# Kernel optimization log

Measured on AMD Instinct MI355X. Metric: run time of the kernel, lower is better.

Reference implementation:

```python
import jax, jax.numpy as jnp
import numpy as np

W_CD = 1.0   # cfg TRAIN.LOSS_WEIGHT_CHAMFER_DISTANCE
W_RV = 1.0   # cfg TRAIN.LOSS_WEIGHT_RANGE_VIEW
W_MASK = 1.0 # cfg TRAIN.LOSS_WEIGHT_MASK


def setup_inputs() -> dict:
    key = jax.random.key(0)
    k0, k1, k2, k3, k4 = jax.random.split(key, 5)
    B, T, H, W = 2, 5, 64, 2048   # batch, future steps, range-image dims
    N = M = 4096                  # n_samples (TEST.N_DOWNSAMPLED_POINTS_CD)
    output_rv = jax.random.normal(k0, (B, T, H, W), jnp.float32)
    mask_logits = jax.random.normal(k1, (B, T, H, W), jnp.float32)
    target_range_image = jax.random.normal(k2, (B, T, H, W), jnp.float32)
    output_points = jax.random.normal(k3, (B, T, N, 3), jnp.float32)
    target_points = jax.random.normal(k4, (B, T, M, 3), jnp.float32)
    return {
        "output_rv": output_rv,
        "mask_logits": mask_logits,
        "output_points": output_points,
        "target_points": target_points,
        "target_range_image": target_range_image,
    }


def _chamfer(output_points, target_points):
    on = jnp.sum(output_points * output_points, axis=-1)            # [B,T,N]
    tn = jnp.sum(target_points * target_points, axis=-1)            # [B,T,M]
    cross = jnp.einsum('btnd,btmd->btnm', output_points, target_points)
    d2 = on[..., :, None] + tn[..., None, :] - 2.0 * cross          # [B,T,N,M]
    dist1 = jnp.min(d2, axis=-1).mean(axis=-1)                      # [B,T] out->tgt NN
    dist2 = jnp.min(d2, axis=-2).mean(axis=-1)                      # [B,T] tgt->out NN
    cd_bt = dist1 + dist2                                           # per (b,s) CD
    return cd_bt.T, jnp.mean(cd_bt)                                 # [T,B] tensor, scalar mean


def reference(output_rv, mask_logits, output_points, target_points, target_range_image):
    # L1 range loss: output values are forced to -1 wherever target == -1
    out_m = jnp.where(target_range_image == -1.0, -1.0, output_rv)
    loss_rv = jnp.mean(jnp.abs(out_m - target_range_image))
    # mask BCE-with-logits: target mask is 1 where range view is valid (> 0)
    tmask = (target_range_image > 0.0).astype(output_rv.dtype)
    x = mask_logits
    loss_mask = jnp.mean(jnp.maximum(x, 0.0) - x * tmask + jnp.log1p(jnp.exp(-jnp.abs(x))))
    # Chamfer distance over fixed-size subsampled point clouds
    cd_tensor, loss_cd = _chamfer(output_points, target_points)
    total = W_CD * loss_cd + W_RV * loss_rv + W_MASK * loss_mask
    return total, cd_tensor, loss_cd, loss_rv, loss_mask
```

## Files before the change

### kernel.cpp

```cpp
#include <hip/hip_runtime.h>
#include <math.h>

#define BB 2
#define TT 5
#define NPTS 4096
#define NBT (BB * TT)
#define NELEM (BB * TT * 64 * 2048)

#define CH_BLOCKS 640
#define QPB 128
#define NQC (NPTS / QPB)
#define CT 1024
#define NT (NPTS / CT)
#define EW_BLOCKS 640

#define EW1 2560
#define EW2 3200

typedef _Float16 h8 __attribute__((ext_vector_type(8)));
typedef float f32x16 __attribute__((ext_vector_type(16)));
typedef float f32x4 __attribute__((ext_vector_type(4)));

__device__ inline unsigned pkh(float a, float b) {
    union { _Float16 h[2]; unsigned u; } c;
    c.h[0] = (_Float16)a;
    c.h[1] = (_Float16)b;
    return c.u;
}

__global__ __launch_bounds__(256) void main_kernel(
        const float4* __restrict__ rv4,
        const float4* __restrict__ lg4,
        const float4* __restrict__ tg4,
        const float* __restrict__ OP,
        const float* __restrict__ TP,
        float* __restrict__ ws) {
    __shared__ __align__(16) uint2 pts[2][CT];
    __shared__ float nqlds[4][32];
    int bid = blockIdx.x;
    int tid = threadIdx.x;
    int lane = tid & 63;
    int wave = tid >> 6;

    if (bid >= CH_BLOCKS) {
        int eb = bid - CH_BLOCKS;
        float srv = 0.0f, smk = 0.0f;
        int base = (eb * 256 + tid) * 2;
#pragma unroll
        for (int u = 0; u < 2; ++u) {
            int i = base + u;
            float4 o4 = rv4[i];
            float4 x4 = lg4[i];
            float4 t4 = tg4[i];
            const float* op = &o4.x;
            const float* xp = &x4.x;
            const float* tp = &t4.x;
#pragma unroll
            for (int j = 0; j < 4; ++j) {
                float tv = tp[j];
                float ov = (tv == -1.0f) ? -1.0f : op[j];
                srv += fabsf(ov - tv);
                float tm = (tv > 0.0f) ? 1.0f : 0.0f;
                float xv = xp[j];
                smk += fmaxf(xv, 0.0f) - xv * tm + __logf(1.0f + __expf(-fabsf(xv)));
            }
        }
#pragma unroll
        for (int off = 32; off > 0; off >>= 1) {
            srv += __shfl_down(srv, off);
            smk += __shfl_down(smk, off);
        }
        __shared__ float s1[4], s2[4];
        if (lane == 0) { s1[wave] = srv; s2[wave] = smk; }
        __syncthreads();
        if (tid == 0) {
            ws[EW1 + eb] = s1[0] + s1[1] + s1[2] + s1[3];
            ws[EW2 + eb] = s2[0] + s2[1] + s2[2] + s2[3];
        }
        return;
    }

    int dir = bid / (NBT * NQC);
    int rem = bid % (NBT * NQC);
    int bt = rem / NQC;
    int qc = rem % NQC;
    const float* P = dir ? TP : OP;
    const float* Q = dir ? OP : TP;
    const float* Pb = P + (size_t)bt * NPTS * 3;
    const float* Qb = Q + (size_t)bt * NPTS * 3;

    int qrow = lane & 31;
    int qidx = qc * QPB + wave * 32 + qrow;
    float qx = 0.0f, qy = 0.0f, qz = 0.0f;
    if (lane < 32) {
        const float* p = Pb + (size_t)qidx * 3;
        qx = p[0]; qy = p[1]; qz = p[2];
        nqlds[wave][qrow] = fmaf(qx, qx, fmaf(qy, qy, qz * qz));
    }
    union { unsigned u[4]; h8 h; } ua;
    ua.u[0] = ua.u[1] = ua.u[2] = ua.u[3] = 0u;
    if (lane < 32) {
        ua.u[0] = pkh(-2.0f * qx, -2.0f * qy);
        ua.u[1] = pkh(-2.0f * qz, 1.0f);
    }
    h8 afrag = ua.h;

    const f32x16 zc = {0.0f, 0.0f, 0.0f, 0.0f, 0.0f, 0.0f, 0.0f, 0.0f,
                       0.0f, 0.0f, 0.0f, 0.0f, 0.0f, 0.0f, 0.0f, 0.0f};
    float vm[16];
#pragma unroll
    for (int r = 0; r < 16; ++r) vm[r] = INFINITY;

#define STAGE(t, b)                                                          \
    {                                                                        \
        int pt0 = (t) * CT + tid * 4;                                        \
        const f32x4* src = (const f32x4*)(Qb + (size_t)pt0 * 3);             \
        f32x4 c0 = src[0], c1 = src[1], c2 = src[2];                         \
        float x0 = c0[0], y0 = c0[1], z0 = c0[2];                            \
        float x1 = c0[3], y1 = c1[0], z1 = c1[1];                            \
        float x2 = c1[2], y2 = c1[3], z2 = c2[0];                            \
        float x3 = c2[1], y3 = c2[2], z3 = c2[3];                            \
        float n0 = fmaf(x0, x0, fmaf(y0, y0, z0 * z0));                      \
        float n1 = fmaf(x1, x1, fmaf(y1, y1, z1 * z1));                      \
        float n2 = fmaf(x2, x2, fmaf(y2, y2, z2 * z2));                      \
        float n3 = fmaf(x3, x3, fmaf(y3, y3, z3 * z3));                      \
        uint4* dst = (uint4*)&pts[b][tid * 4];                               \
        dst[0] = make_uint4(pkh(x0, y0), pkh(z0, n0), pkh(x1, y1), pkh(z1, n1)); \
        dst[1] = make_uint4(pkh(x2, y2), pkh(z2, n2), pkh(x3, y3), pkh(z3, n3)); \
    }

    STAGE(0, 0);
    __syncthreads();
    for (int t = 0; t < NT; ++t) {
        if (t + 1 < NT) STAGE(t + 1, (t + 1) & 1);
        const uint2* pb = pts[t & 1];
#pragma unroll
        for (int g = 0; g < CT / 128; ++g) {
            uint2 b0 = pb[g * 128 + 0 * 32 + qrow];
            uint2 b1 = pb[g * 128 + 1 * 32 + qrow];
            uint2 b2 = pb[g * 128 + 2 * 32 + qrow];
            uint2 b3 = pb[g * 128 + 3 * 32 + qrow];
            union { unsigned u[4]; h8 h; } ub0, ub1, ub2, ub3;
            ub0.u[0] = b0.x; ub0.u[1] = b0.y; ub0.u[2] = 0u; ub0.u[3] = 0u;
            ub1.u[0] = b1.x; ub1.u[1] = b1.y; ub1.u[2] = 0u; ub1.u[3] = 0u;
            ub2.u[0] = b2.x; ub2.u[1] = b2.y; ub2.u[2] = 0u; ub2.u[3] = 0u;
            ub3.u[0] = b3.x; ub3.u[1] = b3.y; ub3.u[2] = 0u; ub3.u[3] = 0u;
            f32x16 d0 = __builtin_amdgcn_mfma_f32_32x32x16_f16(afrag, ub0.h, zc, 0, 0, 0);
            f32x16 d1 = __builtin_amdgcn_mfma_f32_32x32x16_f16(afrag, ub1.h, zc, 0, 0, 0);
            f32x16 d2 = __builtin_amdgcn_mfma_f32_32x32x16_f16(afrag, ub2.h, zc, 0, 0, 0);
            f32x16 d3 = __builtin_amdgcn_mfma_f32_32x32x16_f16(afrag, ub3.h, zc, 0, 0, 0);
#pragma unroll
            for (int r = 0; r < 16; ++r) {
                float a = d0[r], c = d1[r];
                asm("v_min3_f32 %0, %0, %1, %2" : "+v"(vm[r]) : "v"(a), "v"(c));
            }
#pragma unroll
            for (int r = 0; r < 16; ++r) {
                float a = d2[r], c = d3[r];
                asm("v_min3_f32 %0, %0, %1, %2" : "+v"(vm[r]) : "v"(a), "v"(c));
            }
        }
        __syncthreads();
    }

#pragma unroll
    for (int r = 0; r < 16; ++r) {
        float m = vm[r];
        m = fminf(m, __shfl_xor(m, 1));
        m = fminf(m, __shfl_xor(m, 2));
        m = fminf(m, __shfl_xor(m, 4));
        m = fminf(m, __shfl_xor(m, 8));
        m = fminf(m, __shfl_xor(m, 16));
        vm[r] = m;
    }
    float part = 0.0f;
    if ((lane & 31) == 0) {
        int half = lane >> 5;
#pragma unroll
        for (int r = 0; r < 16; ++r) {
            int row = (r & 3) + 8 * (r >> 2) + 4 * half;
            part += vm[r] + nqlds[wave][row];
        }
    }
    part += __shfl_xor(part, 32);
    if (lane == 0) ws[bid * 4 + wave] = part;
}

__global__ void finalize_kernel(const float* __restrict__ ws, float* __restrict__ out) {
    __shared__ float grp[20];
    __shared__ float ra[4], rb[4];
    int tid = threadIdx.x;
    int lane = tid & 63;
    int wave = tid >> 6;

    for (int g = wave; g < 20; g += 4) {
        float s = 0.0f;
        for (int j = lane; j < 128; j += 64) s += ws[g * 128 + j];
#pragma unroll
        for (int off = 32; off > 0; off >>= 1) s += __shfl_down(s, off);
        if (lane == 0) grp[g] = s;
    }

    float sa = 0.0f, sb = 0.0f;
    for (int i = tid; i < EW_BLOCKS; i += 256) {
        sa += ws[EW1 + i];
        sb += ws[EW2 + i];
    }
#pragma unroll
    for (int off = 32; off > 0; off >>= 1) {
        sa += __shfl_down(sa, off);
        sb += __shfl_down(sb, off);
    }
    if (lane == 0) { ra[wave] = sa; rb[wave] = sb; }
    __syncthreads();

    if (tid == 0) {
        const float inv_e = 1.0f / (float)NELEM;
        float loss_rv = (ra[0] + ra[1] + ra[2] + ra[3]) * inv_e;
        float loss_mask = (rb[0] + rb[1] + rb[2] + rb[3]) * inv_e;
        float cd_sum = 0.0f;
        for (int bt = 0; bt < NBT; ++bt) {
            float cd = (grp[bt] + grp[NBT + bt]) * (1.0f / NPTS);
            int b = bt / TT;
            int t = bt % TT;
            out[1 + t * BB + b] = cd;
            cd_sum += cd;
        }
        float loss_cd = cd_sum / (float)NBT;
        out[0] = loss_cd + loss_rv + loss_mask;
        out[11] = loss_cd;
        out[12] = loss_rv;
        out[13] = loss_mask;
    }
}

extern "C" void kernel_launch(void* const* d_in, const int* in_sizes, int n_in,
                              void* d_out, int out_size, void* d_ws, size_t ws_size,
                              hipStream_t stream) {
    const float* output_rv = (const float*)d_in[0];
    const float* mask_logits = (const float*)d_in[1];
    const float* output_points = (const float*)d_in[2];
    const float* target_points = (const float*)d_in[3];
    const float* target_rv = (const float*)d_in[4];
    float* out = (float*)d_out;
    float* ws = (float*)d_ws;

    main_kernel<<<CH_BLOCKS + EW_BLOCKS, 256, 0, stream>>>(
        (const float4*)output_rv, (const float4*)mask_logits,
        (const float4*)target_rv, output_points, target_points, ws);

    finalize_kernel<<<1, 256, 0, stream>>>(ws, out);
}
```

Before: 32.20 us.

## Split chamfer candidates across wave pairs, halve queries per block, reorder blocks

Each chamfer block now handles 64 queries instead of 128. Its four waves form two query groups times two candidate halves, and the whole 4096-point candidate cloud is staged into LDS once instead of double-buffered in tiles. Partial minima from the two candidate halves are merged through shared memory before the block reduction. Elementwise blocks are moved to the front of the grid. The aim is more chamfer blocks for better CU fill and fewer barriers, but each block restages the full candidate set, doubling redundant global loads and packing work, and LDS use rises to 32KB per block.

New measurement: 30.56 us. -5.1%, faster.

```diff
diff --git a/kernel.cpp b/kernel.cpp
--- a/kernel.cpp
+++ b/kernel.cpp
@@ -7,15 +7,13 @@
 #define NBT (BB * TT)
 #define NELEM (BB * TT * 64 * 2048)
 
-#define CH_BLOCKS 640
-#define QPB 128
-#define NQC (NPTS / QPB)
-#define CT 1024
-#define NT (NPTS / CT)
 #define EW_BLOCKS 640
-
-#define EW1 2560
-#define EW2 3200
+#define CH_BLOCKS 1280
+#define QPB 64
+#define NQC 64
+
+#define EW1 1280
+#define EW2 1920
 
 typedef _Float16 h8 __attribute__((ext_vector_type(8)));
 typedef float f32x16 __attribute__((ext_vector_type(16)));
@@ -35,17 +33,17 @@
         const float* __restrict__ OP,
         const float* __restrict__ TP,
         float* __restrict__ ws) {
-    __shared__ __align__(16) uint2 pts[2][CT];
-    __shared__ float nqlds[4][32];
+    __shared__ __align__(16) uint2 pts[4096];
+    __shared__ float nqlds[QPB];
+    __shared__ float qmin[2][QPB];
     int bid = blockIdx.x;
     int tid = threadIdx.x;
     int lane = tid & 63;
     int wave = tid >> 6;
 
-    if (bid >= CH_BLOCKS) {
-        int eb = bid - CH_BLOCKS;
+    if (bid < EW_BLOCKS) {
         float srv = 0.0f, smk = 0.0f;
-        int base = (eb * 256 + tid) * 2;
+        int base = (bid * 256 + tid) * 2;
 #pragma unroll
         for (int u = 0; u < 2; ++u) {
             int i = base + u;
@@ -74,14 +72,15 @@
         if (lane == 0) { s1[wave] = srv; s2[wave] = smk; }
         __syncthreads();
         if (tid == 0) {
-            ws[EW1 + eb] = s1[0] + s1[1] + s1[2] + s1[3];
-            ws[EW2 + eb] = s2[0] + s2[1] + s2[2] + s2[3];
+            ws[EW1 + bid] = s1[0] + s1[1] + s1[2] + s1[3];
+            ws[EW2 + bid] = s2[0] + s2[1] + s2[2] + s2[3];
         }
         return;
     }
 
-    int dir = bid / (NBT * NQC);
-    int rem = bid % (NBT * NQC);
+    int cb = bid - EW_BLOCKS;
+    int dir = cb / (NBT * NQC);
+    int rem = cb % (NBT * NQC);
     int bt = rem / NQC;
     int qc = rem % NQC;
     const float* P = dir ? TP : OP;
@@ -90,12 +89,15 @@
     const float* Qb = Q + (size_t)bt * NPTS * 3;
 
     int qrow = lane & 31;
-    int qidx = qc * QPB + wave * 32 + qrow;
+    int wq = wave & 1;
+    int ph = wave >> 1;
+
+    int qidx = qc * QPB + wq * 32 + qrow;
     float qx = 0.0f, qy = 0.0f, qz = 0.0f;
     if (lane < 32) {
         const float* p = Pb + (size_t)qidx * 3;
         qx = p[0]; qy = p[1]; qz = p[2];
-        nqlds[wave][qrow] = fmaf(qx, qx, fmaf(qy, qy, qz * qz));
+        nqlds[wq * 32 + qrow] = fmaf(qx, qx, fmaf(qy, qy, qz * qz));
     }
     union { unsigned u[4]; h8 h; } ua;
     ua.u[0] = ua.u[1] = ua.u[2] = ua.u[3] = 0u;
@@ -105,62 +107,57 @@
     }
     h8 afrag = ua.h;
 
+#pragma unroll
+    for (int t = 0; t < 4; ++t) {
+        int pt0 = t * 1024 + tid * 4;
+        const f32x4* src = (const f32x4*)(Qb + (size_t)pt0 * 3);
+        f32x4 c0 = src[0], c1 = src[1], c2 = src[2];
+        float x0 = c0[0], y0 = c0[1], z0 = c0[2];
+        float x1 = c0[3], y1 = c1[0], z1 = c1[1];
+        float x2 = c1[2], y2 = c1[3], z2 = c2[0];
+        float x3 = c2[1], y3 = c2[2], z3 = c2[3];
+        float n0 = fmaf(x0, x0, fmaf(y0, y0, z0 * z0));
+        float n1 = fmaf(x1, x1, fmaf(y1, y1, z1 * z1));
+        float n2 = fmaf(x2, x2, fmaf(y2, y2, z2 * z2));
+        float n3 = fmaf(x3, x3, fmaf(y3, y3, z3 * z3));
+        uint4* dst = (uint4*)&pts[t * 1024 + tid * 4];
+        dst[0] = make_uint4(pkh(x0, y0), pkh(z0, n0), pkh(x1, y1), pkh(z1, n1));
+        dst[1] = make_uint4(pkh(x2, y2), pkh(z2, n2), pkh(x3, y3), pkh(z3, n3));
+    }
+    __syncthreads();
+
     const f32x16 zc = {0.0f, 0.0f, 0.0f, 0.0f, 0.0f, 0.0f, 0.0f, 0.0f,
                        0.0f, 0.0f, 0.0f, 0.0f, 0.0f, 0.0f, 0.0f, 0.0f};
     float vm[16];
 #pragma unroll
     for (int r = 0; r < 16; ++r) vm[r] = INFINITY;
 
-#define STAGE(t, b)                                                          \
-    {                                                                        \
-        int pt0 = (t) * CT + tid * 4;                                        \
-        const f32x4* src = (const f32x4*)(Qb + (size_t)pt0 * 3);             \
-        f32x4 c0 = src[0], c1 = src[1], c2 = src[2];                         \
-        float x0 = c0[0], y0 = c0[1], z0 = c0[2];                            \
-        float x1 = c0[3], y1 = c1[0], z1 = c1[1];                            \
-        float x2 = c1[2], y2 = c1[3], z2 = c2[0];                            \
-        float x3 = c2[1], y3 = c2[2], z3 = c2[3];                            \
-        float n0 = fmaf(x0, x0, fmaf(y0, y0, z0 * z0));                      \
-        float n1 = fmaf(x1, x1, fmaf(y1, y1, z1 * z1));                      \
-        float n2 = fmaf(x2, x2, fmaf(y2, y2, z2 * z2));                      \
-        float n3 = fmaf(x3, x3, fmaf(y3, y3, z3 * z3));                      \
-        uint4* dst = (uint4*)&pts[b][tid * 4];                               \
-        dst[0] = make_uint4(pkh(x0, y0), pkh(z0, n0), pkh(x1, y1), pkh(z1, n1)); \
-        dst[1] = make_uint4(pkh(x2, y2), pkh(z2, n2), pkh(x3, y3), pkh(z3, n3)); \
-    }
-
-    STAGE(0, 0);
-    __syncthreads();
-    for (int t = 0; t < NT; ++t) {
-        if (t + 1 < NT) STAGE(t + 1, (t + 1) & 1);
-        const uint2* pb = pts[t & 1];
-#pragma unroll
-        for (int g = 0; g < CT / 128; ++g) {
-            uint2 b0 = pb[g * 128 + 0 * 32 + qrow];
-            uint2 b1 = pb[g * 128 + 1 * 32 + qrow];
-            uint2 b2 = pb[g * 128 + 2 * 32 + qrow];
-            uint2 b3 = pb[g * 128 + 3 * 32 + qrow];
-            union { unsigned u[4]; h8 h; } ub0, ub1, ub2, ub3;
-            ub0.u[0] = b0.x; ub0.u[1] = b0.y; ub0.u[2] = 0u; ub0.u[3] = 0u;
-            ub1.u[0] = b1.x; ub1.u[1] = b1.y; ub1.u[2] = 0u; ub1.u[3] = 0u;
-            ub2.u[0] = b2.x; ub2.u[1] = b2.y; ub2.u[2] = 0u; ub2.u[3] = 0u;
-            ub3.u[0] = b3.x; ub3.u[1] = b3.y; ub3.u[2] = 0u; ub3.u[3] = 0u;
-            f32x16 d0 = __builtin_amdgcn_mfma_f32_32x32x16_f16(afrag, ub0.h, zc, 0, 0, 0);
-            f32x16 d1 = __builtin_amdgcn_mfma_f32_32x32x16_f16(afrag, ub1.h, zc, 0, 0, 0);
-            f32x16 d2 = __builtin_amdgcn_mfma_f32_32x32x16_f16(afrag, ub2.h, zc, 0, 0, 0);
-            f32x16 d3 = __builtin_amdgcn_mfma_f32_32x32x16_f16(afrag, ub3.h, zc, 0, 0, 0);
-#pragma unroll
-            for (int r = 0; r < 16; ++r) {
-                float a = d0[r], c = d1[r];
-                asm("v_min3_f32 %0, %0, %1, %2" : "+v"(vm[r]) : "v"(a), "v"(c));
-            }
-#pragma unroll
-            for (int r = 0; r < 16; ++r) {
-                float a = d2[r], c = d3[r];
-                asm("v_min3_f32 %0, %0, %1, %2" : "+v"(vm[r]) : "v"(a), "v"(c));
-            }
-        }
-        __syncthreads();
+    const uint2* pb = pts + ph * 2048;
+#pragma unroll 4
+    for (int g = 0; g < 16; ++g) {
+        uint2 b0 = pb[g * 128 + 0 * 32 + qrow];
+        uint2 b1 = pb[g * 128 + 1 * 32 + qrow];
+        uint2 b2 = pb[g * 128 + 2 * 32 + qrow];
+        uint2 b3 = pb[g * 128 + 3 * 32 + qrow];
+        union { unsigned u[4]; h8 h; } ub0, ub1, ub2, ub3;
+        ub0.u[0] = b0.x; ub0.u[1] = b0.y; ub0.u[2] = 0u; ub0.u[3] = 0u;
+        ub1.u[0] = b1.x; ub1.u[1] = b1.y; ub1.u[2] = 0u; ub1.u[3] = 0u;
+        ub2.u[0] = b2.x; ub2.u[1] = b2.y; ub2.u[2] = 0u; ub2.u[3] = 0u;
+        ub3.u[0] = b3.x; ub3.u[1] = b3.y; ub3.u[2] = 0u; ub3.u[3] = 0u;
+        f32x16 d0 = __builtin_amdgcn_mfma_f32_32x32x16_f16(afrag, ub0.h, zc, 0, 0, 0);
+        f32x16 d1 = __builtin_amdgcn_mfma_f32_32x32x16_f16(afrag, ub1.h, zc, 0, 0, 0);
+        f32x16 d2 = __builtin_amdgcn_mfma_f32_32x32x16_f16(afrag, ub2.h, zc, 0, 0, 0);
+        f32x16 d3 = __builtin_amdgcn_mfma_f32_32x32x16_f16(afrag, ub3.h, zc, 0, 0, 0);
+#pragma unroll
+        for (int r = 0; r < 16; ++r) {
+            float a = d0[r], c = d1[r];
+            asm("v_min3_f32 %0, %0, %1, %2" : "+v"(vm[r]) : "v"(a), "v"(c));
+        }
+#pragma unroll
+        for (int r = 0; r < 16; ++r) {
+            float a = d2[r], c = d3[r];
+            asm("v_min3_f32 %0, %0, %1, %2" : "+v"(vm[r]) : "v"(a), "v"(c));
+        }
     }
 
 #pragma unroll
@@ -173,17 +170,22 @@
         m = fminf(m, __shfl_xor(m, 16));
         vm[r] = m;
     }
-    float part = 0.0f;
     if ((lane & 31) == 0) {
         int half = lane >> 5;
 #pragma unroll
         for (int r = 0; r < 16; ++r) {
             int row = (r & 3) + 8 * (r >> 2) + 4 * half;
-            part += vm[r] + nqlds[wave][row];
-        }
-    }
-    part += __shfl_xor(part, 32);
-    if (lane == 0) ws[bid * 4 + wave] = part;
+            qmin[ph][wq * 32 + row] = vm[r];
+        }
+    }
+    __syncthreads();
+
+    if (wave == 0) {
+        float m = fminf(qmin[0][lane], qmin[1][lane]) + nqlds[lane];
+#pragma unroll
+        for (int off = 32; off > 0; off >>= 1) m += __shfl_down(m, off);
+        if (lane == 0) ws[cb] = m;
+    }
 }
 
 __global__ void finalize_kernel(const float* __restrict__ ws, float* __restrict__ out) {
@@ -194,8 +196,7 @@
     int wave = tid >> 6;
 
     for (int g = wave; g < 20; g += 4) {
-        float s = 0.0f;
-        for (int j = lane; j < 128; j += 64) s += ws[g * 128 + j];
+        float s = ws[g * 64 + lane];
 #pragma unroll
         for (int off = 32; off > 0; off >>= 1) s += __shfl_down(s, off);
         if (lane == 0) grp[g] = s;
@@ -245,7 +246,7 @@
     float* out = (float*)d_out;
     float* ws = (float*)d_ws;
 
-    main_kernel<<<CH_BLOCKS + EW_BLOCKS, 256, 0, stream>>>(
+    main_kernel<<<EW_BLOCKS + CH_BLOCKS, 256, 0, stream>>>(
         (const float4*)output_rv, (const float4*)mask_logits,
         (const float4*)target_rv, output_points, target_points, ws);
 
```
